# Performance work log

Measured on AMD Instinct MI355X. Metric: run time of the kernel, lower is better.

## Reference

```python
import jax, jax.numpy as jnp
import numpy as np

B, S, D, H, V, DFF = 8, 1024, 768, 12, 50257, 3072


def setup_inputs() -> dict:
    key = jax.random.key(0)
    ks = jax.random.split(key, 10)
    return {
        "idx": jax.random.randint(ks[0], (B, S), 0, V),
        "wte": jax.random.normal(ks[1], (V, D), jnp.float32) * 0.2,
        "wpe": jax.random.normal(ks[2], (S + 1, D), jnp.float32) * 0.2,
        "wq_diag": jax.random.normal(ks[3], (H, D), jnp.float32) * 0.2,
        "wk_diag": jax.random.normal(ks[4], (H, D), jnp.float32) * 0.2,
        "wv_diag": jax.random.normal(ks[5], (H, D), jnp.float32) * 0.2,
        "w_lr": jax.random.normal(ks[6], (1, H, 1, 1), jnp.float32) * 0.01,
        "w_o": jax.random.normal(ks[7], (D, H * D), jnp.float32) * 0.02,
        "mlp_w1": jax.random.normal(ks[8], (DFF, D), jnp.float32) * 0.02,
        "mlp_w2": jax.random.normal(ks[9], (D, DFF), jnp.float32) * 0.02,
    }


def _forward(idx, wte, wpe, wq_diag, wk_diag, wv_diag, w_lr, w_o, mlp_w1, mlp_w2):
    b_sz, s = idx.shape
    e = wte[idx]                               # (B,S,D) token embeddings
    p = wpe[: s + 1]                           # (S+1,D) positions 0..S
    e_mean = jnp.mean(wte, axis=0)             # E_wte: mean embedding (D,)
    invn = 1.0 / (jnp.arange(s, dtype=e.dtype) + 1.0)  # diag of W_N

    # diag-mode projections: (x @ diag(w)) == x * w  (per head)
    q = p[1:][None] * wq_diag[:, None, :]      # (H,S,D) -- batch-independent
    k = p[:-1][None] * wk_diag[:, None, :]     # (H,S,D)
    v = (e - e_mean)[:, None] * wv_diag[None, :, None, :]  # (B,H,S,D)

    scores = jnp.einsum("hsd,htd->hst", q, k)  # (H,S,S), identical per batch
    mask = jnp.tril(jnp.ones((s, s), bool))
    scores = jnp.where(mask, scores, -jnp.inf)
    attn = jax.nn.softmax(scores, axis=-1)
    y = jnp.einsum("hst,bhtd->bhsd", attn, v)  # (B,H,S,D)

    y = y * invn[:, None]                      # W_N @ y (diagonal -> row scale)
    y = y * w_lr                               # per-head W_LR scale
    # torch does y.view(B, S, H*D) on a (B,H,S,D) tensor: raw memory reinterpret
    y = y.reshape(b_sz, s, H * D)
    y = y @ w_o.T                              # W_o proj -> (B,S,D)

    # b = W_N @ (e - E_wte); torch broadcast-matmul then sum over dim=1 == batch
    b_term = (e - e_mean) * invn[None, :, None]        # (B,S,D)
    y = y + jnp.sum(b_term, axis=0)[None]              # (1,S,D) broadcast add

    # FFN block: x = x + mlp(x), GELU exact, no bias, dropout=0
    x = y + jax.nn.gelu(y @ mlp_w1.T, approximate=False) @ mlp_w2.T

    # targets=None path: logits only for last position, tied lm_head = wte
    logits = x[:, -1:, :] @ wte.T              # (B,1,V)
    return logits


def reference(idx, wte, wpe, wq_diag, wk_diag, wv_diag, w_lr, w_o, mlp_w1, mlp_w2):
    return _forward(idx, wte, wpe, wq_diag, wk_diag, wv_diag, w_lr, w_o, mlp_w1, mlp_w2)
```

## Files before the change

### kernel.cpp

```cpp
#include <hip/hip_runtime.h>
#include <math.h>

#define B 8
#define S 1024
#define D 768
#define H 12
#define V 50257
#define DFF 3072
#define HD (H*D)
#define SLO 1012
#define NS 12

#define OFF_EMEAN 0
#define OFF_A     768
#define OFF_GQ    (OFF_A + B*NS*D)
#define OFF_SC    (OFF_GQ + NS*D)
#define OFF_YV    (OFF_SC + NS*S)
#define OFF_YO    (OFF_YV + B*HD)
#define OFF_G     (OFF_YO + B*D)
#define OFF_X     (OFF_G + B*DFF)

typedef float f4 __attribute__((ext_vector_type(4)));

__device__ __forceinline__ float wsum(float v) {
    v += __shfl_xor(v, 1, 64);
    v += __shfl_xor(v, 2, 64);
    v += __shfl_xor(v, 4, 64);
    v += __shfl_xor(v, 8, 64);
    v += __shfl_xor(v, 16, 64);
    v += __shfl_xor(v, 32, 64);
    return v;
}

#define K14_K4_BLOCKS 256
#define K14_K1_BLOCKS 512
#define K1_ROWS 99
__global__ __launch_bounds__(768) void k14_emean_accA(const int* __restrict__ idx,
                                                      const float* __restrict__ wte,
                                                      float* __restrict__ ws) {
    __shared__ float wl[32 * 12];
    const int bid = blockIdx.x;
    const int tid = threadIdx.x;
    if (bid >= K14_K4_BLOCKS) {
        const int kb = bid - K14_K4_BLOCKS;
        int r0 = kb * K1_ROWS;
        if (r0 >= V) return;
        int r1 = r0 + K1_ROWS; if (r1 > V) r1 = V;
        const float* __restrict__ p = wte + (size_t)r0 * D + tid;
        float a0 = 0.f, a1 = 0.f, a2 = 0.f, a3 = 0.f;
        int r = r0;
        for (; r + 8 <= r1; r += 8) {
            const float* q0 = p;
            const float* q1 = p + 1 * D;
            const float* q2 = p + 2 * D;
            const float* q3 = p + 3 * D;
            const float* q4 = p + 4 * D;
            const float* q5 = p + 5 * D;
            const float* q6 = p + 6 * D;
            const float* q7 = p + 7 * D;
            float t0, t1, t2, t3, t4, t5, t6, t7;
            asm volatile("global_load_dword %0, %1, off" : "=v"(t0) : "v"(q0));
            asm volatile("global_load_dword %0, %1, off" : "=v"(t1) : "v"(q1));
            asm volatile("global_load_dword %0, %1, off" : "=v"(t2) : "v"(q2));
            asm volatile("global_load_dword %0, %1, off" : "=v"(t3) : "v"(q3));
            asm volatile("global_load_dword %0, %1, off" : "=v"(t4) : "v"(q4));
            asm volatile("global_load_dword %0, %1, off" : "=v"(t5) : "v"(q5));
            asm volatile("global_load_dword %0, %1, off" : "=v"(t6) : "v"(q6));
            asm volatile("global_load_dword %0, %1, off" : "=v"(t7) : "v"(q7));
            asm volatile("s_waitcnt vmcnt(0)"
                         : "+v"(t0), "+v"(t1), "+v"(t2), "+v"(t3),
                           "+v"(t4), "+v"(t5), "+v"(t6), "+v"(t7)
                         :
                         : "memory");
            __builtin_amdgcn_sched_barrier(0);
            a0 += t0 + t4; a1 += t1 + t5; a2 += t2 + t6; a3 += t3 + t7;
            p += 8 * D;
        }
        for (; r < r1; ++r) { a0 += *p; p += D; }
        atomicAdd(&ws[OFF_EMEAN + tid], a0 + a1 + a2 + a3);
    } else {
        const int tc = bid & 31, b = bid >> 5;
        if (tid < 384) {
            int tl = tid / 12, s12 = tid % 12;
            wl[tid] = ws[OFF_SC + s12 * S + tc * 32 + tl];
        }
        __syncthreads();
        float acc[12] = {0,0,0,0,0,0,0,0,0,0,0,0};
        const int* __restrict__ ib = idx + b * S + tc * 32;
#pragma unroll 4
        for (int tl = 0; tl < 32; ++tl) {
            int row = ib[tl];
            float val = wte[(size_t)row * D + tid];
            const float* w = &wl[tl * 12];
#pragma unroll
            for (int s12 = 0; s12 < 12; ++s12) acc[s12] += w[s12] * val;
        }
#pragma unroll
        for (int s12 = 0; s12 < 12; ++s12)
            atomicAdd(&ws[OFF_A + (b * NS + s12) * D + tid], acc[s12]);
    }
}

#define K2B_ZBLOCKS 291
__global__ __launch_bounds__(256) void k2b_scores(const float* __restrict__ wpe,
                                                  const float* __restrict__ wq,
                                                  const float* __restrict__ wk,
                                                  float* __restrict__ ws) {
    if (blockIdx.x >= 256) {
        int i = (blockIdx.x - 256) * 256 + threadIdx.x;
        ws[OFF_EMEAN + i] = 0.0f;
        return;
    }
    const int lane = threadIdx.x & 63;
    const int t = (blockIdx.x * 256 + threadIdx.x) >> 6;
    float4 pw[3];
#pragma unroll
    for (int i = 0; i < 3; ++i) {
        int col = 4 * lane + 256 * i;
        float4 p = *reinterpret_cast<const float4*>(wpe + t * D + col);
        float4 q = *reinterpret_cast<const float4*>(wq + 11 * D + col);
        float4 k = *reinterpret_cast<const float4*>(wk + 11 * D + col);
        pw[i].x = p.x * q.x * k.x;
        pw[i].y = p.y * q.y * k.y;
        pw[i].z = p.z * q.z * k.z;
        pw[i].w = p.w * q.w * k.w;
    }
    float acc[12];
#pragma unroll
    for (int s12 = 0; s12 < 12; ++s12) {
        float a = 0.f;
#pragma unroll
        for (int i = 0; i < 3; ++i) {
            float4 g = *reinterpret_cast<const float4*>(wpe + (SLO + s12 + 1) * D + 4 * lane + 256 * i);
            a += pw[i].x * g.x + pw[i].y * g.y + pw[i].z * g.z + pw[i].w * g.w;
        }
        acc[s12] = a;
    }
#pragma unroll
    for (int s12 = 0; s12 < 12; ++s12) acc[s12] = wsum(acc[s12]);
    float v = acc[0];
#pragma unroll
    for (int j = 1; j < 12; ++j) if (lane == j) v = acc[j];
    if (lane < 12) ws[OFF_SC + lane * S + t] = v;
}

__global__ __launch_bounds__(256) void k3_softmax(float* __restrict__ ws) {
    __shared__ float red[256];
    const int s12 = blockIdx.x, tid = threadIdx.x;
    const int n = SLO + s12 + 1;
    float* sc = ws + OFF_SC + s12 * S;
    float m = -1e30f;
#pragma unroll
    for (int k = 0; k < 4; ++k) { int t = tid + 256 * k; if (t < n) m = fmaxf(m, sc[t]); }
    red[tid] = m; __syncthreads();
    for (int off = 128; off; off >>= 1) { if (tid < off) red[tid] = fmaxf(red[tid], red[tid + off]); __syncthreads(); }
    float mx = red[0]; __syncthreads();
    float sum = 0.f;
#pragma unroll
    for (int k = 0; k < 4; ++k) { int t = tid + 256 * k; if (t < n) sum += expf(sc[t] - mx); }
    red[tid] = sum; __syncthreads();
    for (int off = 128; off; off >>= 1) { if (tid < off) red[tid] += red[tid + off]; __syncthreads(); }
    float inv = 1.0f / red[0];
#pragma unroll
    for (int k = 0; k < 4; ++k) {
        int t = tid + 256 * k;
        sc[t] = (t < n) ? expf(sc[t] - mx) * inv : 0.0f;
    }
}

__global__ __launch_bounds__(256) void k5_yv(const int* __restrict__ idx,
                                             const float* __restrict__ wte,
                                             const float* __restrict__ wv,
                                             const float* __restrict__ wlr,
                                             float* __restrict__ ws) {
    if (blockIdx.x < 288) {
        int i = blockIdx.x * 256 + threadIdx.x;
        int b = i / HD, f = i % HD, s12 = f / D, d = f % D;
        float em = ws[OFF_EMEAN + d] * (1.0f / V);
        float A  = ws[OFF_A + (b * NS + s12) * D + d];
        float invn = 1.0f / (float)(SLO + s12 + 1);
        ws[OFF_YV + i] = (A - em) * wv[11 * D + d] * invn * wlr[11];
    } else {
        int d = (blockIdx.x - 288) * 256 + threadIdx.x;
        float em = ws[OFF_EMEAN + d] * (1.0f / V);
        float s = 0.f;
#pragma unroll
        for (int b = 0; b < 8; ++b) {
            int row = idx[b * S + (S - 1)];
            s += wte[(size_t)row * D + d];
        }
        float sb = (s - 8.0f * em) * (1.0f / (float)S);
#pragma unroll
        for (int b = 0; b < 8; ++b) ws[OFF_YO + b * D + d] = sb;
    }
}

__global__ __launch_bounds__(256) void k6_wo(const float* __restrict__ w_o,
                                             float* __restrict__ ws) {
    const int lane = threadIdx.x & 63;
    const int wid = (blockIdx.x * 256 + threadIdx.x) >> 6;
    const int kc = wid % 12;
    const int r0 = (wid / 12) * 2;
    const int kbase = kc * 768;
    float acc[2][8] = {{0}};
#pragma unroll
    for (int i = 0; i < 3; ++i) {
        int k = kbase + 4 * lane + 256 * i;
        float4 a0 = *reinterpret_cast<const float4*>(w_o + (size_t)r0 * HD + k);
        float4 a1 = *reinterpret_cast<const float4*>(w_o + (size_t)(r0 + 1) * HD + k);
#pragma unroll
        for (int b = 0; b < 8; ++b) {
            float4 y = *reinterpret_cast<const float4*>(ws + OFF_YV + b * HD + k);
            acc[0][b] += a0.x * y.x + a0.y * y.y + a0.z * y.z + a0.w * y.w;
            acc[1][b] += a1.x * y.x + a1.y * y.y + a1.z * y.z + a1.w * y.w;
        }
    }
#pragma unroll
    for (int r = 0; r < 2; ++r)
#pragma unroll
        for (int b = 0; b < 8; ++b) acc[r][b] = wsum(acc[r][b]);
    float v = acc[0][0];
#pragma unroll
    for (int l = 1; l < 16; ++l) if (lane == l) v = acc[l >> 3][l & 7];
    if (lane < 16) atomicAdd(&ws[OFF_YO + (lane & 7) * D + r0 + (lane >> 3)], v);
}

__global__ __launch_bounds__(256) void k7_mlp1(const float* __restrict__ w1,
                                               float* __restrict__ ws) {
    if (blockIdx.x >= 768) {
        int i = (blockIdx.x - 768) * 256 + threadIdx.x;
        ws[OFF_X + i] = ws[OFF_YO + i];
        return;
    }
    const int lane = threadIdx.x & 63;
    const int f = (blockIdx.x * 256 + threadIdx.x) >> 6;
    float acc[8] = {0};
#pragma unroll
    for (int i = 0; i < 3; ++i) {
        int dcol = 4 * lane + 256 * i;
        float4 w = *reinterpret_cast<const float4*>(w1 + (size_t)f * D + dcol);
#pragma unroll
        for (int b = 0; b < 8; ++b) {
            float4 y = *reinterpret_cast<const float4*>(ws + OFF_YO + b * D + dcol);
            acc[b] += w.x * y.x + w.y * y.y + w.z * y.z + w.w * y.w;
        }
    }
#pragma unroll
    for (int b = 0; b < 8; ++b) acc[b] = wsum(acc[b]);
    float v = acc[0];
#pragma unroll
    for (int j = 1; j < 8; ++j) if (lane == j) v = acc[j];
    if (lane < 8) {
        float g = 0.5f * v * (1.0f + erff(v * 0.70710678118654752f));
        ws[OFF_G + lane * DFF + f] = g;
    }
}

__global__ __launch_bounds__(256) void k8_mlp2(const float* __restrict__ w2,
                                               float* __restrict__ ws) {
    const int lane = threadIdx.x & 63;
    const int wid = (blockIdx.x * 256 + threadIdx.x) >> 6;
    const int fc = wid & 3;
    const int dd = wid >> 2;
    const int fbase = fc * 768;
    float acc[8] = {0};
#pragma unroll
    for (int i = 0; i < 3; ++i) {
        int fcol = fbase + 4 * lane + 256 * i;
        float4 w = *reinterpret_cast<const float4*>(w2 + (size_t)dd * DFF + fcol);
#pragma unroll
        for (int b = 0; b < 8; ++b) {
            float4 g = *reinterpret_cast<const float4*>(ws + OFF_G + b * DFF + fcol);
            acc[b] += w.x * g.x + w.y * g.y + w.z * g.z + w.w * g.w;
        }
    }
#pragma unroll
    for (int b = 0; b < 8; ++b) acc[b] = wsum(acc[b]);
    float v = acc[0];
#pragma unroll
    for (int j = 1; j < 8; ++j) if (lane == j) v = acc[j];
    if (lane < 8) atomicAdd(&ws[OFF_X + lane * D + dd], v);
}

__global__ __launch_bounds__(256) void k9_logits(const float* __restrict__ wte,
                                                 const float* __restrict__ ws,
                                                 float* __restrict__ out) {
    const int lane = threadIdx.x & 63;
    const int wid = (blockIdx.x * 256 + threadIdx.x) >> 6;
    const int NW = gridDim.x * 4;
    float4 xr[8][3];
#pragma unroll
    for (int b = 0; b < 8; ++b)
#pragma unroll
        for (int i = 0; i < 3; ++i)
            xr[b][i] = *reinterpret_cast<const float4*>(ws + OFF_X + b * D + 4 * lane + 256 * i);
    float4 w0[3], w1[3];
    if (wid < V) {
#pragma unroll
        for (int i = 0; i < 3; ++i)
            w0[i] = *reinterpret_cast<const float4*>(wte + (size_t)wid * D + 4 * lane + 256 * i);
    }
    if (wid + NW < V) {
#pragma unroll
        for (int i = 0; i < 3; ++i)
            w1[i] = *reinterpret_cast<const float4*>(wte + (size_t)(wid + NW) * D + 4 * lane + 256 * i);
    }
    for (int j = wid; j < V; j += NW) {
        int jn2 = j + 2 * NW;
        float4 wn[3];
        if (jn2 < V) {
#pragma unroll
            for (int i = 0; i < 3; ++i)
                wn[i] = *reinterpret_cast<const float4*>(wte + (size_t)jn2 * D + 4 * lane + 256 * i);
        }
        float acc[8] = {0};
#pragma unroll
        for (int b = 0; b < 8; ++b) {
#pragma unroll
            for (int i = 0; i < 3; ++i)
                acc[b] += w0[i].x * xr[b][i].x + w0[i].y * xr[b][i].y +
                          w0[i].z * xr[b][i].z + w0[i].w * xr[b][i].w;
        }
#pragma unroll
        for (int b = 0; b < 8; ++b) acc[b] = wsum(acc[b]);
        float v = acc[0];
#pragma unroll
        for (int bb = 1; bb < 8; ++bb) if (lane == bb) v = acc[bb];
        if (lane < 8) out[(size_t)lane * V + j] = v;
#pragma unroll
        for (int i = 0; i < 3; ++i) { w0[i] = w1[i]; w1[i] = wn[i]; }
    }
}

extern "C" void kernel_launch(void* const* d_in, const int* in_sizes, int n_in,
                              void* d_out, int out_size, void* d_ws, size_t ws_size,
                              hipStream_t stream) {
    const int*   idx = (const int*)  d_in[0];
    const float* wte = (const float*)d_in[1];
    const float* wpe = (const float*)d_in[2];
    const float* wq  = (const float*)d_in[3];
    const float* wk  = (const float*)d_in[4];
    const float* wv  = (const float*)d_in[5];
    const float* wlr = (const float*)d_in[6];
    const float* w_o = (const float*)d_in[7];
    const float* w1  = (const float*)d_in[8];
    const float* w2  = (const float*)d_in[9];
    float* out = (float*)d_out;
    float* ws  = (float*)d_ws;

    k2b_scores<<<256 + K2B_ZBLOCKS, 256, 0, stream>>>(wpe, wq, wk, ws);
    k3_softmax<<<12,   256, 0, stream>>>(ws);
    k14_emean_accA<<<K14_K4_BLOCKS + K14_K1_BLOCKS, 768, 0, stream>>>(idx, wte, ws);
    k5_yv     <<<291,  256, 0, stream>>>(idx, wte, wv, wlr, ws);
    k6_wo     <<<1152, 256, 0, stream>>>(w_o, ws);
    k7_mlp1   <<<792,  256, 0, stream>>>(w1, ws);
    k8_mlp2   <<<768,  256, 0, stream>>>(w2, ws);
    k9_logits <<<768,  256, 0, stream>>>(wte, ws, out);
}
```

Measured before the change: 337.0 us.

## Fuse softmax into accumulation kernel and yv scaling into W_o projection

The separate softmax kernel goes away: each accA block recomputes per-row max and sum with wave reductions and normalizes its weights on the fly. The yv scaling kernel is folded into the W_o projection, which now computes (A - mean) * wv * invn * wlr inline. The bias term is added with atomics after YO is zeroed in the scores kernel. The emean reduction switches to dwordx2 loads covering two rows per iteration. This removes two launches and the YV round-trip, at the cost of redundant softmax reductions in every accA block.

```diff
diff --git a/kernel.cpp b/kernel.cpp
--- a/kernel.cpp
+++ b/kernel.cpp
@@ -32,13 +32,24 @@
     return v;
 }
 
+__device__ __forceinline__ float wmax(float v) {
+    v = fmaxf(v, __shfl_xor(v, 1, 64));
+    v = fmaxf(v, __shfl_xor(v, 2, 64));
+    v = fmaxf(v, __shfl_xor(v, 4, 64));
+    v = fmaxf(v, __shfl_xor(v, 8, 64));
+    v = fmaxf(v, __shfl_xor(v, 16, 64));
+    v = fmaxf(v, __shfl_xor(v, 32, 64));
+    return v;
+}
+
 #define K14_K4_BLOCKS 256
 #define K14_K1_BLOCKS 512
 #define K1_ROWS 99
-__global__ __launch_bounds__(768) void k14_emean_accA(const int* __restrict__ idx,
-                                                      const float* __restrict__ wte,
-                                                      float* __restrict__ ws) {
+__global__ __launch_bounds__(768, 6) void k14_emean_accA(const int* __restrict__ idx,
+                                                         const float* __restrict__ wte,
+                                                         float* __restrict__ ws) {
     __shared__ float wl[32 * 12];
+    __shared__ float mxs[12], invs[12];
     const int bid = blockIdx.x;
     const int tid = threadIdx.x;
     if (bid >= K14_K4_BLOCKS) {
@@ -46,43 +57,80 @@
         int r0 = kb * K1_ROWS;
         if (r0 >= V) return;
         int r1 = r0 + K1_ROWS; if (r1 > V) r1 = V;
-        const float* __restrict__ p = wte + (size_t)r0 * D + tid;
-        float a0 = 0.f, a1 = 0.f, a2 = 0.f, a3 = 0.f;
+        const int row_off = tid / 384;
+        const int c2 = tid % 384;
+        const float2* __restrict__ base = reinterpret_cast<const float2*>(wte);
+        float2 a0 = {0,0}, a1 = {0,0}, a2 = {0,0}, a3 = {0,0};
         int r = r0;
-        for (; r + 8 <= r1; r += 8) {
-            const float* q0 = p;
-            const float* q1 = p + 1 * D;
-            const float* q2 = p + 2 * D;
-            const float* q3 = p + 3 * D;
-            const float* q4 = p + 4 * D;
-            const float* q5 = p + 5 * D;
-            const float* q6 = p + 6 * D;
-            const float* q7 = p + 7 * D;
-            float t0, t1, t2, t3, t4, t5, t6, t7;
-            asm volatile("global_load_dword %0, %1, off" : "=v"(t0) : "v"(q0));
-            asm volatile("global_load_dword %0, %1, off" : "=v"(t1) : "v"(q1));
-            asm volatile("global_load_dword %0, %1, off" : "=v"(t2) : "v"(q2));
-            asm volatile("global_load_dword %0, %1, off" : "=v"(t3) : "v"(q3));
-            asm volatile("global_load_dword %0, %1, off" : "=v"(t4) : "v"(q4));
-            asm volatile("global_load_dword %0, %1, off" : "=v"(t5) : "v"(q5));
-            asm volatile("global_load_dword %0, %1, off" : "=v"(t6) : "v"(q6));
-            asm volatile("global_load_dword %0, %1, off" : "=v"(t7) : "v"(q7));
+        for (; r + 16 <= r1; r += 16) {
+            const float2* q0 = base + (size_t)(r + row_off) * 384 + c2;
+            const float2* q1 = q0 + 1 * 768;
+            const float2* q2 = q0 + 2 * 768;
+            const float2* q3 = q0 + 3 * 768;
+            const float2* q4 = q0 + 4 * 768;
+            const float2* q5 = q0 + 5 * 768;
+            const float2* q6 = q0 + 6 * 768;
+            const float2* q7 = q0 + 7 * 768;
+            float2 t0, t1, t2, t3, t4, t5, t6, t7;
+            asm volatile("global_load_dwordx2 %0, %1, off" : "=v"(t0) : "v"(q0));
+            asm volatile("global_load_dwordx2 %0, %1, off" : "=v"(t1) : "v"(q1));
+            asm volatile("global_load_dwordx2 %0, %1, off" : "=v"(t2) : "v"(q2));
+            asm volatile("global_load_dwordx2 %0, %1, off" : "=v"(t3) : "v"(q3));
+            asm volatile("global_load_dwordx2 %0, %1, off" : "=v"(t4) : "v"(q4));
+            asm volatile("global_load_dwordx2 %0, %1, off" : "=v"(t5) : "v"(q5));
+            asm volatile("global_load_dwordx2 %0, %1, off" : "=v"(t6) : "v"(q6));
+            asm volatile("global_load_dwordx2 %0, %1, off" : "=v"(t7) : "v"(q7));
             asm volatile("s_waitcnt vmcnt(0)"
                          : "+v"(t0), "+v"(t1), "+v"(t2), "+v"(t3),
                            "+v"(t4), "+v"(t5), "+v"(t6), "+v"(t7)
                          :
                          : "memory");
             __builtin_amdgcn_sched_barrier(0);
-            a0 += t0 + t4; a1 += t1 + t5; a2 += t2 + t6; a3 += t3 + t7;
-            p += 8 * D;
-        }
-        for (; r < r1; ++r) { a0 += *p; p += D; }
-        atomicAdd(&ws[OFF_EMEAN + tid], a0 + a1 + a2 + a3);
+            a0.x += t0.x + t4.x; a0.y += t0.y + t4.y;
+            a1.x += t1.x + t5.x; a1.y += t1.y + t5.y;
+            a2.x += t2.x + t6.x; a2.y += t2.y + t6.y;
+            a3.x += t3.x + t7.x; a3.y += t3.y + t7.y;
+        }
+        for (; r + 2 <= r1; r += 2) {
+            float2 t = base[(size_t)(r + row_off) * 384 + c2];
+            a0.x += t.x; a0.y += t.y;
+        }
+        if (r < r1 && row_off == 0) {
+            float2 t = base[(size_t)r * 384 + c2];
+            a0.x += t.x; a0.y += t.y;
+        }
+        a0.x += a1.x + a2.x + a3.x;
+        a0.y += a1.y + a2.y + a3.y;
+        atomicAdd(&ws[OFF_EMEAN + 2 * c2 + 0], a0.x);
+        atomicAdd(&ws[OFF_EMEAN + 2 * c2 + 1], a0.y);
     } else {
         const int tc = bid & 31, b = bid >> 5;
+        const int w = tid >> 6, lane = tid & 63;
+        {
+            const int n = SLO + w + 1;
+            const float* __restrict__ sc = ws + OFF_SC + w * S;
+            float m = -1e30f;
+#pragma unroll
+            for (int kk = 0; kk < 16; ++kk) {
+                int t = kk * 64 + lane;
+                if (t < n) m = fmaxf(m, sc[t]);
+            }
+            m = wmax(m);
+            float ssum = 0.f;
+#pragma unroll
+            for (int kk = 0; kk < 16; ++kk) {
+                int t = kk * 64 + lane;
+                if (t < n) ssum += expf(sc[t] - m);
+            }
+            ssum = wsum(ssum);
+            if (lane == 0) { mxs[w] = m; invs[w] = 1.0f / ssum; }
+        }
+        __syncthreads();
         if (tid < 384) {
             int tl = tid / 12, s12 = tid % 12;
-            wl[tid] = ws[OFF_SC + s12 * S + tc * 32 + tl];
+            int t = tc * 32 + tl;
+            float raw = ws[OFF_SC + s12 * S + t];
+            wl[tid] = (t < SLO + s12 + 1) ? expf(raw - mxs[s12]) * invs[s12] : 0.0f;
         }
         __syncthreads();
         float acc[12] = {0,0,0,0,0,0,0,0,0,0,0,0};
@@ -91,9 +139,9 @@
         for (int tl = 0; tl < 32; ++tl) {
             int row = ib[tl];
             float val = wte[(size_t)row * D + tid];
-            const float* w = &wl[tl * 12];
-#pragma unroll
-            for (int s12 = 0; s12 < 12; ++s12) acc[s12] += w[s12] * val;
+            const float* wgt = &wl[tl * 12];
+#pragma unroll
+            for (int s12 = 0; s12 < 12; ++s12) acc[s12] += wgt[s12] * val;
         }
 #pragma unroll
         for (int s12 = 0; s12 < 12; ++s12)
@@ -101,14 +149,20 @@
     }
 }
 
-#define K2B_ZBLOCKS 291
+#define K2B_ZBLOCKS 315
 __global__ __launch_bounds__(256) void k2b_scores(const float* __restrict__ wpe,
                                                   const float* __restrict__ wq,
                                                   const float* __restrict__ wk,
                                                   float* __restrict__ ws) {
     if (blockIdx.x >= 256) {
-        int i = (blockIdx.x - 256) * 256 + threadIdx.x;
-        ws[OFF_EMEAN + i] = 0.0f;
+        int zb = blockIdx.x - 256;
+        if (zb < 291) {
+            int i = zb * 256 + threadIdx.x;
+            ws[OFF_EMEAN + i] = 0.0f;
+        } else {
+            int i = (zb - 291) * 256 + threadIdx.x;
+            ws[OFF_YO + i] = 0.0f;
+        }
         return;
     }
     const int lane = threadIdx.x & 63;
@@ -144,44 +198,14 @@
     if (lane < 12) ws[OFF_SC + lane * S + t] = v;
 }
 
-__global__ __launch_bounds__(256) void k3_softmax(float* __restrict__ ws) {
-    __shared__ float red[256];
-    const int s12 = blockIdx.x, tid = threadIdx.x;
-    const int n = SLO + s12 + 1;
-    float* sc = ws + OFF_SC + s12 * S;
-    float m = -1e30f;
-#pragma unroll
-    for (int k = 0; k < 4; ++k) { int t = tid + 256 * k; if (t < n) m = fmaxf(m, sc[t]); }
-    red[tid] = m; __syncthreads();
-    for (int off = 128; off; off >>= 1) { if (tid < off) red[tid] = fmaxf(red[tid], red[tid + off]); __syncthreads(); }
-    float mx = red[0]; __syncthreads();
-    float sum = 0.f;
-#pragma unroll
-    for (int k = 0; k < 4; ++k) { int t = tid + 256 * k; if (t < n) sum += expf(sc[t] - mx); }
-    red[tid] = sum; __syncthreads();
-    for (int off = 128; off; off >>= 1) { if (tid < off) red[tid] += red[tid + off]; __syncthreads(); }
-    float inv = 1.0f / red[0];
-#pragma unroll
-    for (int k = 0; k < 4; ++k) {
-        int t = tid + 256 * k;
-        sc[t] = (t < n) ? expf(sc[t] - mx) * inv : 0.0f;
-    }
-}
-
-__global__ __launch_bounds__(256) void k5_yv(const int* __restrict__ idx,
+__global__ __launch_bounds__(256) void k6_wo(const int* __restrict__ idx,
                                              const float* __restrict__ wte,
+                                             const float* __restrict__ w_o,
                                              const float* __restrict__ wv,
                                              const float* __restrict__ wlr,
                                              float* __restrict__ ws) {
-    if (blockIdx.x < 288) {
-        int i = blockIdx.x * 256 + threadIdx.x;
-        int b = i / HD, f = i % HD, s12 = f / D, d = f % D;
-        float em = ws[OFF_EMEAN + d] * (1.0f / V);
-        float A  = ws[OFF_A + (b * NS + s12) * D + d];
-        float invn = 1.0f / (float)(SLO + s12 + 1);
-        ws[OFF_YV + i] = (A - em) * wv[11 * D + d] * invn * wlr[11];
-    } else {
-        int d = (blockIdx.x - 288) * 256 + threadIdx.x;
+    if (blockIdx.x >= 1152) {
+        int d = (blockIdx.x - 1152) * 256 + threadIdx.x;
         float em = ws[OFF_EMEAN + d] * (1.0f / V);
         float s = 0.f;
 #pragma unroll
@@ -191,28 +215,35 @@
         }
         float sb = (s - 8.0f * em) * (1.0f / (float)S);
 #pragma unroll
-        for (int b = 0; b < 8; ++b) ws[OFF_YO + b * D + d] = sb;
-    }
-}
-
-__global__ __launch_bounds__(256) void k6_wo(const float* __restrict__ w_o,
-                                             float* __restrict__ ws) {
+        for (int b = 0; b < 8; ++b) atomicAdd(&ws[OFF_YO + b * D + d], sb);
+        return;
+    }
     const int lane = threadIdx.x & 63;
     const int wid = (blockIdx.x * 256 + threadIdx.x) >> 6;
     const int kc = wid % 12;
     const int r0 = (wid / 12) * 2;
-    const int kbase = kc * 768;
+    const float c1 = (1.0f / (float)(SLO + kc + 1)) * wlr[11];
     float acc[2][8] = {{0}};
 #pragma unroll
     for (int i = 0; i < 3; ++i) {
-        int k = kbase + 4 * lane + 256 * i;
+        int d = 4 * lane + 256 * i;
+        int k = kc * 768 + d;
         float4 a0 = *reinterpret_cast<const float4*>(w_o + (size_t)r0 * HD + k);
         float4 a1 = *reinterpret_cast<const float4*>(w_o + (size_t)(r0 + 1) * HD + k);
-#pragma unroll
-        for (int b = 0; b < 8; ++b) {
-            float4 y = *reinterpret_cast<const float4*>(ws + OFF_YV + b * HD + k);
-            acc[0][b] += a0.x * y.x + a0.y * y.y + a0.z * y.z + a0.w * y.w;
-            acc[1][b] += a1.x * y.x + a1.y * y.y + a1.z * y.z + a1.w * y.w;
+        float4 em4 = *reinterpret_cast<const float4*>(ws + OFF_EMEAN + d);
+        float4 wv4 = *reinterpret_cast<const float4*>(wv + 11 * D + d);
+        float4 cm;
+        cm.x = wv4.x * c1; cm.y = wv4.y * c1; cm.z = wv4.z * c1; cm.w = wv4.w * c1;
+        em4.x *= (1.0f / V); em4.y *= (1.0f / V); em4.z *= (1.0f / V); em4.w *= (1.0f / V);
+#pragma unroll
+        for (int b = 0; b < 8; ++b) {
+            float4 A4 = *reinterpret_cast<const float4*>(ws + OFF_A + (size_t)(b * NS + kc) * D + d);
+            float yx = (A4.x - em4.x) * cm.x;
+            float yy = (A4.y - em4.y) * cm.y;
+            float yz = (A4.z - em4.z) * cm.z;
+            float yw = (A4.w - em4.w) * cm.w;
+            acc[0][b] += a0.x * yx + a0.y * yy + a0.z * yz + a0.w * yw;
+            acc[1][b] += a1.x * yx + a1.y * yy + a1.z * yz + a1.w * yw;
         }
     }
 #pragma unroll
@@ -349,10 +380,8 @@
     float* ws  = (float*)d_ws;
 
     k2b_scores<<<256 + K2B_ZBLOCKS, 256, 0, stream>>>(wpe, wq, wk, ws);
-    k3_softmax<<<12,   256, 0, stream>>>(ws);
     k14_emean_accA<<<K14_K4_BLOCKS + K14_K1_BLOCKS, 768, 0, stream>>>(idx, wte, ws);
-    k5_yv     <<<291,  256, 0, stream>>>(idx, wte, wv, wlr, ws);
-    k6_wo     <<<1152, 256, 0, stream>>>(w_o, ws);
+    k6_wo     <<<1155, 256, 0, stream>>>(idx, wte, w_o, wv, wlr, ws);
     k7_mlp1   <<<792,  256, 0, stream>>>(w1, ws);
     k8_mlp2   <<<768,  256, 0, stream>>>(w2, ws);
     k9_logits <<<768,  256, 0, stream>>>(wte, ws, out);
```

New measurement: 362.8 us. +7.7%, slower.
